# Kernel tuning notes

Measured on AMD Instinct MI355X. Metric: run time of the kernel, lower is better.

The kernel has to match this reference:

```python
import jax, jax.numpy as jnp
import numpy as np

PATCH = 32
K_FILT = 4
B, NP, C = 32, 256, 3


def _dct_matrix(n):
    i = np.arange(n)[:, None]
    j = np.arange(n)[None, :]
    scale = np.where(i == 0, np.sqrt(1.0 / n), np.sqrt(2.0 / n))
    m = scale * np.cos((j + 0.5) * np.pi * i / n)
    return jnp.asarray(m, dtype=jnp.float32)


def _bandpass_filters(n, k_filt):
    i = np.arange(n)[:, None]
    j = np.arange(n)[None, :]
    s = i + j  # [n, n]
    ks = np.arange(k_filt)[:, None, None]
    lo = 2.0 * n / k_filt * ks
    hi = 2.0 * n / k_filt * (ks + 1)
    f = ((s >= lo) & (s < hi)).astype(np.float32)  # [K, n, n]
    return jnp.asarray(f)


def setup_inputs() -> dict:
    key = jax.random.key(0)
    x = jax.random.normal(key, (B, NP, C, PATCH, PATCH), dtype=jnp.float32)
    return {
        'x': x,
        'dct_matrix': _dct_matrix(PATCH),
        'bandpass_filters': _bandpass_filters(PATCH, K_FILT),
    }


def reference(x, dct_matrix, bandpass_filters):
    # Batched 2D DCT: D @ patch @ D^T for every (b, n, c) patch.
    dct_coeffs = jnp.einsum('ih,bnchw,jw->bncij', dct_matrix, x, dct_matrix)
    log_abs = jnp.log1p(jnp.abs(dct_coeffs))  # log(|X| + 1)
    # patch_score = sum_k sum_c 2^k * (log_abs[c] * filter_k).sum()
    k_weights = 2.0 ** jnp.arange(bandpass_filters.shape[0], dtype=jnp.float32)
    weight_map = jnp.einsum('k,khw->hw', k_weights, bandpass_filters)  # [H, W]
    patch_grades = jnp.einsum('bnchw,hw->bn', log_abs, weight_map)
    return dct_coeffs, patch_grades
```

## Files before the change

### kernel.cpp

```cpp
#include <hip/hip_runtime.h>

#define CH   3
#define WPB  4
#define BLK  (WPB * 64)
#define SPW  3
#define ZST  36

typedef __attribute__((ext_vector_type(8))) short bf16x8;
typedef __attribute__((ext_vector_type(4))) float f32x4;

static __device__ __forceinline__ unsigned bf16_rne(float f) {
    unsigned u = __float_as_uint(f);
    u += 0x7FFF + ((u >> 16) & 1);
    return u >> 16;
}
static __device__ __forceinline__ unsigned split2pk(float f) {
    unsigned hu = bf16_rne(f);
    float hf = __uint_as_float(hu << 16);
    unsigned lu = bf16_rne(f - hf);
    return (lu << 16) | hu;
}

__global__ __launch_bounds__(BLK) void dct_grade_kernel(
    const float* __restrict__ x,
    const float* __restrict__ dct,
    float* __restrict__ out_coeffs,
    float* __restrict__ out_grades)
{
    __shared__ __align__(16) unsigned Z[WPB][32 * ZST];

    const int tid  = threadIdx.x;
    const int wid  = tid >> 6;
    const int lane = tid & 63;
    const int g    = lane >> 4;
    const int r    = lane & 15;
    const int swz  = (r & 3) << 3;

    bf16x8 dh[2], dl[2];
    #pragma unroll
    for (int nt = 0; nt < 2; ++nt) {
        const float* dp = dct + (r + nt * 16) * 32 + g * 8;
        float4 v0 = *reinterpret_cast<const float4*>(dp);
        float4 v1 = *reinterpret_cast<const float4*>(dp + 4);
        float vv[8] = {v0.x, v0.y, v0.z, v0.w, v1.x, v1.y, v1.z, v1.w};
        #pragma unroll
        for (int j = 0; j < 8; ++j) {
            unsigned pk = split2pk(vv[j]);
            dh[nt][j] = (short)(pk & 0xFFFFu);
            dl[nt][j] = (short)(pk >> 16);
        }
    }

    unsigned* Zw = &Z[wid][0];
    const int sbase = (blockIdx.x * WPB + wid) * SPW;
    float gpatch = 0.0f;

    for (int s = 0; s < SPW; ++s) {
        const int sg = sbase + s;
        const float* xg   = x          + (size_t)sg * 1024;
        float*       outp = out_coeffs + (size_t)sg * 1024;

        bf16x8 xh[2], xl[2];
        #pragma unroll
        for (int mt = 0; mt < 2; ++mt) {
            const float* xb = xg + (8 * g) * 32 + r + mt * 16;
            float xv[8];
            #pragma unroll
            for (int j = 0; j < 8; ++j) xv[j] = xb[j * 32];
            #pragma unroll
            for (int j = 0; j < 8; ++j) {
                unsigned pk = split2pk(xv[j]);
                xh[mt][j] = (short)(pk & 0xFFFFu);
                xl[mt][j] = (short)(pk >> 16);
            }
        }

        f32x4 a1[2][2];
        #pragma unroll
        for (int mt = 0; mt < 2; ++mt)
            #pragma unroll
            for (int nt = 0; nt < 2; ++nt) {
                f32x4 acc = {0.f, 0.f, 0.f, 0.f};
                acc = __builtin_amdgcn_mfma_f32_16x16x32_bf16(xh[mt], dh[nt], acc, 0, 0, 0);
                acc = __builtin_amdgcn_mfma_f32_16x16x32_bf16(xh[mt], dl[nt], acc, 0, 0, 0);
                acc = __builtin_amdgcn_mfma_f32_16x16x32_bf16(xl[mt], dh[nt], acc, 0, 0, 0);
                a1[mt][nt] = acc;
            }

        #pragma unroll
        for (int mt = 0; mt < 2; ++mt)
            #pragma unroll
            for (int nt = 0; nt < 2; ++nt)
                #pragma unroll
                for (int q = 0; q < 4; ++q) {
                    unsigned pk = split2pk(a1[mt][nt][q]);
                    int i = r + nt * 16;
                    int w = 4 * g + q + mt * 16;
                    Zw[i * ZST + (w ^ swz)] = pk;
                }

        bf16x8 zh2[2], zl2[2];
        #pragma unroll
        for (int mt2 = 0; mt2 < 2; ++mt2) {
            const int i2 = r + mt2 * 16;
            const unsigned* zp = Zw + i2 * ZST + ((8 * g) ^ swz);
            uint4 u0 = *reinterpret_cast<const uint4*>(zp);
            uint4 u1 = *reinterpret_cast<const uint4*>(zp + 4);
            unsigned uu[8] = {u0.x, u0.y, u0.z, u0.w, u1.x, u1.y, u1.z, u1.w};
            #pragma unroll
            for (int j = 0; j < 8; ++j) {
                zh2[mt2][j] = (short)(uu[j] & 0xFFFFu);
                zl2[mt2][j] = (short)(uu[j] >> 16);
            }
        }

        f32x4 y[2][2];
        #pragma unroll
        for (int mt2 = 0; mt2 < 2; ++mt2)
            #pragma unroll
            for (int nt = 0; nt < 2; ++nt) {
                f32x4 acc = {0.f, 0.f, 0.f, 0.f};
                acc = __builtin_amdgcn_mfma_f32_16x16x32_bf16(zh2[mt2], dh[nt], acc, 0, 0, 0);
                acc = __builtin_amdgcn_mfma_f32_16x16x32_bf16(zh2[mt2], dl[nt], acc, 0, 0, 0);
                acc = __builtin_amdgcn_mfma_f32_16x16x32_bf16(zl2[mt2], dh[nt], acc, 0, 0, 0);
                y[mt2][nt] = acc;
            }

        #pragma unroll
        for (int mt2 = 0; mt2 < 2; ++mt2)
            #pragma unroll
            for (int nt = 0; nt < 2; ++nt)
                #pragma unroll
                for (int q = 0; q < 4; ++q) {
                    float yv = y[mt2][nt][q];
                    int row = 4 * g + q + mt2 * 16;
                    int col = r + nt * 16;
                    outp[row * 32 + col] = yv;
                    float wgt = (float)(1 << ((row + col) >> 4));
                    gpatch = fmaf(__logf(1.0f + fabsf(yv)), wgt, gpatch);
                }
    }

    #pragma unroll
    for (int off = 32; off; off >>= 1)
        gpatch += __shfl_xor(gpatch, off);
    if (lane == 0)
        out_grades[sbase / 3] = gpatch;
}

extern "C" void kernel_launch(void* const* d_in, const int* in_sizes, int n_in,
                              void* d_out, int out_size, void* d_ws, size_t ws_size,
                              hipStream_t stream) {
    const float* x   = (const float*)d_in[0];
    const float* dct = (const float*)d_in[1];
    float* out_coeffs = (float*)d_out;
    float* out_grades = (float*)d_out + (size_t)8192 * CH * 1024;

    const int n_slices = 8192 * CH;
    const int grid = n_slices / (WPB * SPW);
    dct_grade_kernel<<<grid, BLK, 0, stream>>>(x, dct, out_coeffs, out_grades);
}
```

Baseline: 185.9 us.

## Prefetch next slice, use hardware bf16 pack converts, split hi/lo LDS planes

Loads of the next slice's input are issued before the current slice is processed, so global load latency overlaps the MFMA work. The software bf16 round-and-split is replaced with the packed v_cvt_pk_bf16_f32 instruction, and the intermediate is stored as separate high and low bf16 planes in LDS, which lets it be written with vector stores and read back as bf16x8 directly without unpacking. The epilogue uses log2 with precomputed weights and scales by ln2 once at the end, and launch bounds request 4 blocks per SM. The cost is higher register pressure from holding two slices of input, plus reliance on an inline-asm instruction that is specific to this architecture.

```diff
diff --git a/kernel.cpp b/kernel.cpp
--- a/kernel.cpp
+++ b/kernel.cpp
@@ -4,37 +4,35 @@
 #define WPB  4
 #define BLK  (WPB * 64)
 #define SPW  3
-#define ZST  36
+#define ZSTW 20
 
 typedef __attribute__((ext_vector_type(8))) short bf16x8;
 typedef __attribute__((ext_vector_type(4))) float f32x4;
 
-static __device__ __forceinline__ unsigned bf16_rne(float f) {
-    unsigned u = __float_as_uint(f);
-    u += 0x7FFF + ((u >> 16) & 1);
-    return u >> 16;
-}
-static __device__ __forceinline__ unsigned split2pk(float f) {
-    unsigned hu = bf16_rne(f);
-    float hf = __uint_as_float(hu << 16);
-    unsigned lu = bf16_rne(f - hf);
-    return (lu << 16) | hu;
+union U8 { bf16x8 v; unsigned w[4]; uint4 q; };
+
+static __device__ __forceinline__ uint2 split2x(float f0, float f1) {
+    unsigned hpk, lpk;
+    asm("v_cvt_pk_bf16_f32 %0, %1, %2" : "=v"(hpk) : "v"(f0), "v"(f1));
+    float r0 = f0 - __uint_as_float(hpk << 16);
+    float r1 = f1 - __uint_as_float(hpk & 0xFFFF0000u);
+    asm("v_cvt_pk_bf16_f32 %0, %1, %2" : "=v"(lpk) : "v"(r0), "v"(r1));
+    return make_uint2(hpk, lpk);
 }
 
-__global__ __launch_bounds__(BLK) void dct_grade_kernel(
+__global__ __launch_bounds__(BLK, 4) void dct_grade_kernel(
     const float* __restrict__ x,
     const float* __restrict__ dct,
     float* __restrict__ out_coeffs,
     float* __restrict__ out_grades)
 {
-    __shared__ __align__(16) unsigned Z[WPB][32 * ZST];
+    __shared__ __align__(16) unsigned Zp[WPB][2][32 * ZSTW];
 
     const int tid  = threadIdx.x;
     const int wid  = tid >> 6;
     const int lane = tid & 63;
     const int g    = lane >> 4;
     const int r    = lane & 15;
-    const int swz  = (r & 3) << 3;
 
     bf16x8 dh[2], dl[2];
     #pragma unroll
@@ -43,39 +41,49 @@
         float4 v0 = *reinterpret_cast<const float4*>(dp);
         float4 v1 = *reinterpret_cast<const float4*>(dp + 4);
         float vv[8] = {v0.x, v0.y, v0.z, v0.w, v1.x, v1.y, v1.z, v1.w};
+        U8 H, L;
         #pragma unroll
-        for (int j = 0; j < 8; ++j) {
-            unsigned pk = split2pk(vv[j]);
-            dh[nt][j] = (short)(pk & 0xFFFFu);
-            dl[nt][j] = (short)(pk >> 16);
+        for (int k = 0; k < 4; ++k) {
+            uint2 p = split2x(vv[2 * k], vv[2 * k + 1]);
+            H.w[k] = p.x; L.w[k] = p.y;
         }
+        dh[nt] = H.v; dl[nt] = L.v;
     }
 
-    unsigned* Zw = &Z[wid][0];
+    const int base = 4 * g + r;
+    float wq[4];
+    #pragma unroll
+    for (int q = 0; q < 4; ++q)
+        wq[q] = (base + q >= 16) ? 2.0f : 1.0f;
+
+    unsigned* Zh = &Zp[wid][0][0];
+    unsigned* Zl = &Zp[wid][1][0];
     const int sbase = (blockIdx.x * WPB + wid) * SPW;
     float gpatch = 0.0f;
 
-    for (int s = 0; s < SPW; ++s) {
-        const int sg = sbase + s;
-        const float* xg   = x          + (size_t)sg * 1024;
-        float*       outp = out_coeffs + (size_t)sg * 1024;
+    auto loadX = [&](float (&xv)[2][8], int sg) {
+        const float* xg = x + (size_t)sg * 1024;
+        #pragma unroll
+        for (int mt = 0; mt < 2; ++mt) {
+            const float* xb = xg + (8 * g) * 32 + r + 16 * mt;
+            #pragma unroll
+            for (int j = 0; j < 8; ++j) xv[mt][j] = xb[j * 32];
+        }
+    };
 
+    auto processSlice = [&](const float (&xv)[2][8], int sg) {
         bf16x8 xh[2], xl[2];
         #pragma unroll
         for (int mt = 0; mt < 2; ++mt) {
-            const float* xb = xg + (8 * g) * 32 + r + mt * 16;
-            float xv[8];
+            U8 H, L;
             #pragma unroll
-            for (int j = 0; j < 8; ++j) xv[j] = xb[j * 32];
-            #pragma unroll
-            for (int j = 0; j < 8; ++j) {
-                unsigned pk = split2pk(xv[j]);
-                xh[mt][j] = (short)(pk & 0xFFFFu);
-                xl[mt][j] = (short)(pk >> 16);
+            for (int k = 0; k < 4; ++k) {
+                uint2 p = split2x(xv[mt][2 * k], xv[mt][2 * k + 1]);
+                H.w[k] = p.x; L.w[k] = p.y;
             }
+            xh[mt] = H.v; xl[mt] = L.v;
         }
 
-        f32x4 a1[2][2];
         #pragma unroll
         for (int mt = 0; mt < 2; ++mt)
             #pragma unroll
@@ -84,37 +92,25 @@
                 acc = __builtin_amdgcn_mfma_f32_16x16x32_bf16(xh[mt], dh[nt], acc, 0, 0, 0);
                 acc = __builtin_amdgcn_mfma_f32_16x16x32_bf16(xh[mt], dl[nt], acc, 0, 0, 0);
                 acc = __builtin_amdgcn_mfma_f32_16x16x32_bf16(xl[mt], dh[nt], acc, 0, 0, 0);
-                a1[mt][nt] = acc;
+                uint2 p01 = split2x(acc[0], acc[1]);
+                uint2 p23 = split2x(acc[2], acc[3]);
+                const int i  = r + nt * 16;
+                const int wp = 2 * g + 8 * mt;
+                *reinterpret_cast<uint2*>(Zh + i * ZSTW + wp) = make_uint2(p01.x, p23.x);
+                *reinterpret_cast<uint2*>(Zl + i * ZSTW + wp) = make_uint2(p01.y, p23.y);
             }
-
-        #pragma unroll
-        for (int mt = 0; mt < 2; ++mt)
-            #pragma unroll
-            for (int nt = 0; nt < 2; ++nt)
-                #pragma unroll
-                for (int q = 0; q < 4; ++q) {
-                    unsigned pk = split2pk(a1[mt][nt][q]);
-                    int i = r + nt * 16;
-                    int w = 4 * g + q + mt * 16;
-                    Zw[i * ZST + (w ^ swz)] = pk;
-                }
 
         bf16x8 zh2[2], zl2[2];
         #pragma unroll
         for (int mt2 = 0; mt2 < 2; ++mt2) {
             const int i2 = r + mt2 * 16;
-            const unsigned* zp = Zw + i2 * ZST + ((8 * g) ^ swz);
-            uint4 u0 = *reinterpret_cast<const uint4*>(zp);
-            uint4 u1 = *reinterpret_cast<const uint4*>(zp + 4);
-            unsigned uu[8] = {u0.x, u0.y, u0.z, u0.w, u1.x, u1.y, u1.z, u1.w};
-            #pragma unroll
-            for (int j = 0; j < 8; ++j) {
-                zh2[mt2][j] = (short)(uu[j] & 0xFFFFu);
-                zl2[mt2][j] = (short)(uu[j] >> 16);
-            }
+            U8 H, L;
+            H.q = *reinterpret_cast<const uint4*>(Zh + i2 * ZSTW + 4 * g);
+            L.q = *reinterpret_cast<const uint4*>(Zl + i2 * ZSTW + 4 * g);
+            zh2[mt2] = H.v; zl2[mt2] = L.v;
         }
 
-        f32x4 y[2][2];
+        float* outp = out_coeffs + (size_t)sg * 1024;
         #pragma unroll
         for (int mt2 = 0; mt2 < 2; ++mt2)
             #pragma unroll
@@ -123,29 +119,31 @@
                 acc = __builtin_amdgcn_mfma_f32_16x16x32_bf16(zh2[mt2], dh[nt], acc, 0, 0, 0);
                 acc = __builtin_amdgcn_mfma_f32_16x16x32_bf16(zh2[mt2], dl[nt], acc, 0, 0, 0);
                 acc = __builtin_amdgcn_mfma_f32_16x16x32_bf16(zl2[mt2], dh[nt], acc, 0, 0, 0);
-                y[mt2][nt] = acc;
-            }
-
-        #pragma unroll
-        for (int mt2 = 0; mt2 < 2; ++mt2)
-            #pragma unroll
-            for (int nt = 0; nt < 2; ++nt)
+                float* op = outp + (4 * g + 16 * mt2) * 32 + (r + 16 * nt);
+                const float ws = (float)(1 << (mt2 + nt));
                 #pragma unroll
                 for (int q = 0; q < 4; ++q) {
-                    float yv = y[mt2][nt][q];
-                    int row = 4 * g + q + mt2 * 16;
-                    int col = r + nt * 16;
-                    outp[row * 32 + col] = yv;
-                    float wgt = (float)(1 << ((row + col) >> 4));
-                    gpatch = fmaf(__logf(1.0f + fabsf(yv)), wgt, gpatch);
+                    float yv = acc[q];
+                    op[q * 32] = yv;
+                    float lg = __log2f(1.0f + fabsf(yv));
+                    gpatch = fmaf(lg, wq[q] * ws, gpatch);
                 }
-    }
+            }
+    };
+
+    float xA[2][8], xB[2][8];
+    loadX(xA, sbase + 0);
+    loadX(xB, sbase + 1);
+    processSlice(xA, sbase + 0);
+    loadX(xA, sbase + 2);
+    processSlice(xB, sbase + 1);
+    processSlice(xA, sbase + 2);
 
     #pragma unroll
     for (int off = 32; off; off >>= 1)
         gpatch += __shfl_xor(gpatch, off);
     if (lane == 0)
-        out_grades[sbase / 3] = gpatch;
+        out_grades[sbase / 3] = gpatch * 0.6931471805599453f;
 }
 
 extern "C" void kernel_launch(void* const* d_in, const int* in_sizes, int n_in,
```

Result: faster. 182.2 us (-2.0%).
